# Kernel optimization log

Measured on AMD Instinct MI355X. Metric: run time of the kernel, lower is better.

## Reference

```python
import jax, jax.numpy as jnp
import numpy as np

BATCH, QLEN, KVLEN = 4, 8, 512
C, H = 512, 8
N = C // H  # 64
D_W, D_A, D_V, D_G = 32, 32, 32, 96
GN_EPS = 1e-5 * 8 ** 2  # head_size_divisor = 8


def setup_inputs() -> dict:
    key = jax.random.key(0)
    ks = jax.random.split(key, 32)
    rn = lambda i, sh, s=1.0: jax.random.normal(ks[i], sh, dtype=jnp.float32) * s
    ru = lambda i, sh: jax.random.uniform(ks[i], sh, dtype=jnp.float32)
    s = C ** -0.5
    return {
        "query": rn(0, (BATCH, QLEN, C)),
        "keyval": rn(1, (BATCH, KVLEN, C)),
        "v_first": rn(2, (BATCH * QLEN, KVLEN, C)),
        "x_r": ru(3, (1, 1, C)), "x_w": ru(4, (1, 1, C)), "x_k": ru(5, (1, 1, C)),
        "x_v": ru(6, (1, 1, C)), "x_a": ru(7, (1, 1, C)), "x_g": ru(8, (1, 1, C)),
        "w0": jnp.linspace(-7.0, -2.0, C, dtype=jnp.float32).reshape(1, 1, C) + 0.5,
        "w1": rn(9, (C, D_W), 0.02), "w2": rn(10, (D_W, C), 0.02),
        "a0": rn(11, (1, 1, C), 0.01), "a1": rn(12, (C, D_A), 0.02), "a2": rn(13, (D_A, C), 0.02),
        "v0": jnp.ones((1, 1, C), jnp.float32), "v1": rn(14, (C, D_V), 0.02), "v2": rn(15, (D_V, C), 0.02),
        "g1": rn(16, (C, D_G), 0.02), "g2": rn(17, (D_G, C), 0.02),
        "k_k": 0.85 + rn(18, (1, 1, C), 0.02), "k_a": jnp.ones((1, 1, C), jnp.float32),
        "r_k": rn(19, (H, N), 0.02),
        "Wr": rn(20, (C, C), 0.5 * s), "Wk": rn(21, (C, C), 0.05 * s),
        "Wv": rn(22, (C, C), 0.5 * s), "Wo": rn(23, (C, C), s),
        "ln_w": 1.0 + rn(24, (C,), 0.02), "ln_b": rn(25, (C,), 0.02),
    }


def _rwkv7_scan(r, w, k, v, a, b):
    # r,w,k,v,a,b: [B,T,C]; RWKV7 generalized delta rule, state [B,H,N,N] (value x key).
    B, T, _ = r.shape
    toTBHN = lambda t: t.reshape(B, T, H, N).transpose(1, 0, 2, 3)  # [T,B,H,N]
    rT, kT, vT, aT, bT = map(toTBHN, (r, k, v, a, b))
    wT = jnp.exp(-jnp.exp(toTBHN(w)))  # decay in (0,1)

    def step(state, xs):
        r_t, w_t, k_t, v_t, a_t, b_t = xs
        sa = jnp.einsum('bhij,bhj->bhi', state, a_t)  # state @ a
        state = (state * w_t[:, :, None, :]
                 + sa[..., None] * b_t[:, :, None, :]
                 + v_t[..., None] * k_t[:, :, None, :])
        out = jnp.einsum('bhij,bhj->bhi', state, r_t)
        return state, out

    state0 = jnp.zeros((B, H, N, N), dtype=jnp.float32)
    _, outs = jax.lax.scan(step, state0, (rT, wT, kT, vT, aT, bT))
    return outs.transpose(1, 0, 2, 3).reshape(B, T, C)  # [B,T,C]


def _forward(query, keyval, v_first, x_r, x_w, x_k, x_v, x_a, x_g,
             w0, w1, w2, a0, a1, a2, v0, v1, v2, g1, g2,
             k_k, k_a, r_k, Wr, Wk, Wv, Wo, ln_w, ln_b):
    batch, qlen, Cc = query.shape
    kvlen = keyval.shape[1]
    # cross-product expansion: every (query token, keyval sequence) pair
    eq = jnp.repeat(query[:, :, None, :], kvlen, axis=2).reshape(-1, kvlen, Cc)
    ek = jnp.repeat(keyval[:, None, :, :], qlen, axis=1).reshape(-1, kvlen, Cc)
    B, T = ek.shape[0], kvlen
    xx_cross = eq - ek
    shifted = jnp.pad(ek, ((0, 0), (1, 0), (0, 0)))[:, :-1]  # time_shift
    xx_kv = shifted - ek
    x = ek
    xr = x + xx_cross * x_r
    xw = x + xx_cross * x_w
    xa = x + xx_cross * x_a
    xg = x + xx_cross * x_g
    xk = x + xx_kv * x_k
    xv = x + xx_kv * x_v

    r = xr @ Wr
    w = -jax.nn.softplus(-(w0 + jnp.tanh(xw @ w1) @ w2)) - 0.5
    k = xk @ Wk
    v = xv @ Wv
    v = v + (v_first - v) * jax.nn.sigmoid(v0 + (xv @ v1) @ v2)  # layer_id != 0
    a = jax.nn.sigmoid(a0 + (xa @ a1) @ a2)
    g = jax.nn.sigmoid(xg @ g1) @ g2

    kk = k * k_k
    kkh = kk.reshape(B, T, H, N)
    kkh = kkh / jnp.maximum(jnp.linalg.norm(kkh, axis=-1, keepdims=True), 1e-12)
    kk = kkh.reshape(B, T, Cc)
    k = k * (1.0 + (a - 1.0) * k_a)

    xo = _rwkv7_scan(r, w, k, v, -kk, kk * a)

    # GroupNorm over H groups of N channels, eps = 1e-5 * head_size_divisor^2
    y = xo.reshape(B * T, H, N)
    mu = y.mean(axis=-1, keepdims=True)
    var = y.var(axis=-1, keepdims=True)
    yn = (y - mu) * jax.lax.rsqrt(var + GN_EPS)
    xo = (yn.reshape(B * T, Cc) * ln_w + ln_b).reshape(B, T, Cc)

    rk = (r.reshape(B, T, H, N) * k.reshape(B, T, H, N) * r_k).sum(axis=-1, keepdims=True)
    xo = xo + (rk * v.reshape(B, T, H, N)).reshape(B, T, Cc)
    xo = xo * g
    xo = xo[:, -1, :]  # frames=None path
    xo = xo.reshape(batch, qlen, Cc) @ Wo
    return xo, v_first


def reference(query, keyval, v_first, x_r, x_w, x_k, x_v, x_a, x_g,
              w0, w1, w2, a0, a1, a2, v0, v1, v2, g1, g2,
              k_k, k_a, r_k, Wr, Wk, Wv, Wo, ln_w, ln_b):
    return _forward(query, keyval, v_first, x_r, x_w, x_k, x_v, x_a, x_g,
                    w0, w1, w2, a0, a1, a2, v0, v1, v2, g1, g2,
                    k_k, k_a, r_k, Wr, Wk, Wv, Wo, ln_w, ln_b)
```

## Files before the change

### kernel.cpp

```cpp
#include <hip/hip_runtime.h>
#include <cstdint>

#define TT 512
#define CC 512
#define HH 8
#define NN 64
#define BQ 32
#define NB 4
#define TG 128

__device__ __forceinline__ float sigm(float x){ return 1.f/(1.f+__expf(-x)); }

__device__ __forceinline__ float wsum(float x){
  #pragma unroll
  for (int o=32;o;o>>=1) x += __shfl_xor(x, o, 64);
  return x;
}

template<int NR>
__device__ __forceinline__ void rowsum64_batch(float* x){
  #pragma unroll
  for (int i=0;i<NR;i++)
    x[i] += __int_as_float(__builtin_amdgcn_mov_dpp(__float_as_int(x[i]), 0x121, 0xf, 0xf, true));
  #pragma unroll
  for (int i=0;i<NR;i++)
    x[i] += __int_as_float(__builtin_amdgcn_mov_dpp(__float_as_int(x[i]), 0x122, 0xf, 0xf, true));
  #pragma unroll
  for (int i=0;i<NR;i++)
    x[i] += __int_as_float(__builtin_amdgcn_mov_dpp(__float_as_int(x[i]), 0x124, 0xf, 0xf, true));
  #pragma unroll
  for (int i=0;i<NR;i++)
    x[i] += __int_as_float(__builtin_amdgcn_mov_dpp(__float_as_int(x[i]), 0x128, 0xf, 0xf, true));
  float y[NR];
  #pragma unroll
  for (int i=0;i<NR;i++) asm("v_mov_b32 %0, %1" : "=v"(y[i]) : "v"(x[i]));
  #pragma unroll
  for (int i=0;i<NR;i++) asm("v_permlane16_swap_b32 %0, %1" : "+v"(x[i]), "+v"(y[i]));
  #pragma unroll
  for (int i=0;i<NR;i++) x[i] += y[i];
  #pragma unroll
  for (int i=0;i<NR;i++) asm("v_mov_b32 %0, %1" : "=v"(y[i]) : "v"(x[i]));
  #pragma unroll
  for (int i=0;i<NR;i++) asm("v_permlane32_swap_b32 %0, %1" : "+v"(x[i]), "+v"(y[i]));
  #pragma unroll
  for (int i=0;i<NR;i++) x[i] += y[i];
}

__global__ __launch_bounds__(256) void k_prep(
  const float* __restrict__ q, const float* __restrict__ kv,
  const float* __restrict__ x_r, const float* __restrict__ x_w,
  const float* __restrict__ x_a, const float* __restrict__ x_g,
  const float* __restrict__ w1, const float* __restrict__ a1,
  const float* __restrict__ g1,
  float* __restrict__ Qw, float* __restrict__ Qa,
  float* __restrict__ ghw, float* __restrict__ xrw)
{
  int bq = blockIdx.x, b = bq >> 3, tid = threadIdx.x;
  int wave = tid >> 6, lane = tid & 63;
  __shared__ float qxw[CC], qxa[CC], sxg[CC];
  for (int c = tid; c < CC; c += 256){
    float qv = q[bq*CC + c];
    float kl = kv[((size_t)b*TT + (TT-1))*CC + c];
    xrw[bq*CC + c] = kl + (qv - kl)*x_r[c];
    sxg[c] = kl + (qv - kl)*x_g[c];
    qxw[c] = qv*x_w[c];
    qxa[c] = qv*x_a[c];
  }
  __syncthreads();
  for (int dot = wave; dot < 160; dot += 4){
    const float* buf; const float* W; int ld, dd;
    if (dot < 32)      { buf = qxw; W = w1; ld = 32; dd = dot; }
    else if (dot < 64) { buf = qxa; W = a1; ld = 32; dd = dot-32; }
    else               { buf = sxg; W = g1; ld = 96; dd = dot-64; }
    float s = 0.f;
    #pragma unroll
    for (int m = 0; m < 8; m++){
      int c = m*64 + lane;
      s = fmaf(buf[c], W[c*ld + dd], s);
    }
    s = wsum(s);
    if (lane == 0){
      if (dot < 32)      Qw[bq*32 + dd] = s;
      else if (dot < 64) Qa[bq*32 + dd] = s;
      else               ghw[bq*96 + dd] = sigm(s);
    }
  }
}

__global__ __launch_bounds__(256) void k_rg(
  const float* __restrict__ xrw, const float* __restrict__ ghw,
  const float* __restrict__ Wr, const float* __restrict__ g2,
  float* __restrict__ rrow, float* __restrict__ grow)
{
  int bq = blockIdx.y; int co0 = blockIdx.x*64;
  int tid = threadIdx.x, tx = tid & 63, ty = tid >> 6;
  __shared__ float sxr[CC];
  __shared__ float sgh[96];
  __shared__ float red[4][64];
  sxr[tid]     = xrw[bq*CC + tid];
  sxr[tid+256] = xrw[bq*CC + tid + 256];
  if (tid < 96) sgh[tid] = ghw[bq*96 + tid];
  __syncthreads();
  float p = 0.f;
  for (int i = 0; i < 128; i++){
    int c = ty*128 + i;
    p = fmaf(sxr[c], Wr[(size_t)c*CC + co0 + tx], p);
  }
  red[ty][tx] = p;
  float pg = 0.f;
  for (int d = ty*24; d < ty*24 + 24; d++)
    pg = fmaf(sgh[d], g2[(size_t)d*CC + co0 + tx], pg);
  __syncthreads();
  if (ty == 0)
    rrow[bq*CC + co0 + tx] = (red[0][tx]+red[1][tx])+(red[2][tx]+red[3][tx]);
  __syncthreads();
  red[ty][tx] = pg;
  __syncthreads();
  if (ty == 0)
    grow[bq*CC + co0 + tx] = (red[0][tx]+red[1][tx])+(red[2][tx]+red[3][tx]);
}

__global__ __launch_bounds__(256) void k_shift(
  const float* __restrict__ kv, const float* __restrict__ x_k,
  const float* __restrict__ x_v,
  float* __restrict__ xk, float* __restrict__ xv)
{
  int g = blockIdx.x*256 + threadIdx.x;
  int bt = g >> 7, t = bt & (TT-1), c4 = g & 127;
  const float4* kv4 = (const float4*)kv;
  float4 cur = kv4[g];
  float4 sh  = t ? kv4[g-128] : make_float4(0.f,0.f,0.f,0.f);
  float4 kc  = ((const float4*)x_k)[c4];
  float4 vc  = ((const float4*)x_v)[c4];
  float4 ok, ov;
  ok.x = cur.x + (sh.x-cur.x)*kc.x; ov.x = cur.x + (sh.x-cur.x)*vc.x;
  ok.y = cur.y + (sh.y-cur.y)*kc.y; ov.y = cur.y + (sh.y-cur.y)*vc.y;
  ok.z = cur.z + (sh.z-cur.z)*kc.z; ov.z = cur.z + (sh.z-cur.z)*vc.z;
  ok.w = cur.w + (sh.w-cur.w)*kc.w; ov.w = cur.w + (sh.w-cur.w)*vc.w;
  ((float4*)xk)[g] = ok;
  ((float4*)xv)[g] = ov;
}

__global__ __launch_bounds__(256) void k_pgemm(
  const float* __restrict__ kv, const float* __restrict__ xv,
  const float* __restrict__ x_w, const float* __restrict__ x_a,
  const float* __restrict__ w1, const float* __restrict__ a1,
  const float* __restrict__ v1,
  float* __restrict__ Pw, float* __restrict__ Pa, float* __restrict__ HV)
{
  int mat = blockIdx.y;
  int r0 = blockIdx.x * 64;
  const float* A = (mat == 2) ? xv : kv;
  const float* B = (mat == 0) ? w1 : (mat == 1) ? a1 : v1;
  float* O       = (mat == 0) ? Pw : (mat == 1) ? Pa : HV;
  int tid = threadIdx.x;
  __shared__ float As[32][65];
  __shared__ float Bs[32][32];
  __shared__ float scl[CC];
  for (int c = tid; c < CC; c += 256)
    scl[c] = (mat == 0) ? (1.f - x_w[c]) : (mat == 1) ? (1.f - x_a[c]) : 1.f;
  __syncthreads();
  int tx = tid & 31, ty = tid >> 5;
  float acc[8];
  #pragma unroll
  for (int i = 0; i < 8; i++) acc[i] = 0.f;
  for (int k0 = 0; k0 < 512; k0 += 32){
    #pragma unroll
    for (int p = 0; p < 8; p++){
      int e = tid + p*256;
      int kk2 = e & 31, r = e >> 5;
      As[kk2][r] = A[(size_t)(r0+r)*512 + k0 + kk2] * scl[k0 + kk2];
    }
    #pragma unroll
    for (int p = 0; p < 4; p++){
      int e = tid + p*256;
      int n = e & 31, kk2 = e >> 5;
      Bs[kk2][n] = B[(size_t)(k0+kk2)*32 + n];
    }
    __syncthreads();
    #pragma unroll
    for (int kk2 = 0; kk2 < 32; kk2++){
      float bb = Bs[kk2][tx];
      #pragma unroll
      for (int i = 0; i < 8; i++)
        acc[i] = fmaf(As[kk2][ty*8 + i], bb, acc[i]);
    }
    __syncthreads();
  }
  #pragma unroll
  for (int i = 0; i < 8; i++)
    O[(size_t)(r0 + ty*8 + i)*32 + tx] = acc[i];
}

__global__ __launch_bounds__(256) void gemm2(
  const float* __restrict__ A0, const float* __restrict__ W0, float* __restrict__ kgP,
  const float* __restrict__ A1, const float* __restrict__ W1, float* __restrict__ vpP)
{
  __shared__ float As[32][68];
  __shared__ float Bs[32][64];
  int z = blockIdx.z;
  const float* A = z ? A1 : A0;
  const float* W = z ? W1 : W0;
  int tid = threadIdx.x;
  int tx = tid & 15, ty = tid >> 4;
  int m0 = blockIdx.y*64, n0 = blockIdx.x*64;
  float acc[4][4];
  #pragma unroll
  for (int i=0;i<4;i++)
    #pragma unroll
    for (int j=0;j<4;j++) acc[i][j]=0.f;

  for (int k0 = 0; k0 < 512; k0 += 32){
    #pragma unroll
    for (int i = 0; i < 8; i++){
      int e = tid + i*256;
      int kk = e & 31, m = e >> 5;
      As[kk][m] = A[(size_t)(m0+m)*512 + k0 + kk];
    }
    #pragma unroll
    for (int i = 0; i < 8; i++){
      int e = tid + i*256;
      int n = e & 63, kk = e >> 6;
      Bs[kk][n] = W[(size_t)(k0+kk)*512 + n0 + n];
    }
    __syncthreads();
    #pragma unroll
    for (int kk = 0; kk < 32; kk++){
      float a4[4], b4[4];
      #pragma unroll
      for (int i=0;i<4;i++) a4[i] = As[kk][ty*4+i];
      #pragma unroll
      for (int j=0;j<4;j++) b4[j] = Bs[kk][tx*4+j];
      #pragma unroll
      for (int i=0;i<4;i++)
        #pragma unroll
        for (int j=0;j<4;j++) acc[i][j] += a4[i]*b4[j];
    }
    __syncthreads();
  }
  int m = m0 + ty*4;
  int b = m >> 9, t = m & (TT-1), tg = t >> 2;
  int h = n0 >> 6;
  float* dstB = z ? vpP : kgP;
  float4* dst = (float4*)dstB + ((size_t)(b*HH + h)*TG + tg)*64 + tx*4;
  #pragma unroll
  for (int j=0;j<4;j++)
    dst[j] = make_float4(acc[0][j],acc[1][j],acc[2][j],acc[3][j]);
}

__global__ __launch_bounds__(512) void k_svn(
  const float* __restrict__ HV, const float* __restrict__ v2,
  const float* __restrict__ v0, const float* __restrict__ k_k,
  const float* __restrict__ kgP,
  float* __restrict__ svP, float* __restrict__ kkP)
{
  int blk = blockIdx.x;
  int b = blk >> 7, tg = blk & (TG-1);
  int tid = threadIdx.x;
  __shared__ float hv[4][32];
  if (tid < 128){
    int u = tid >> 5, d = tid & 31;
    hv[u][d] = HV[((size_t)(b*TT + tg*4 + u))*32 + d];
  }
  __syncthreads();
  int c = tid, h = c >> 6, cc0 = c & 63;
  size_t o = ((size_t)(b*HH + h)*TG + tg)*64 + cc0;
  float4 kg4 = ((const float4*)kgP)[o];
  float kkc = k_k[c];
  float q0 = kg4.x*kkc, q1 = kg4.y*kkc, q2 = kg4.z*kkc, q3 = kg4.w*kkc;
  float ss[4] = {q0*q0, q1*q1, q2*q2, q3*q3};
  rowsum64_batch<4>(ss);
  float4 kkq;
  kkq.x = q0 / fmaxf(sqrtf(ss[0]), 1e-12f);
  kkq.y = q1 / fmaxf(sqrtf(ss[1]), 1e-12f);
  kkq.z = q2 / fmaxf(sqrtf(ss[2]), 1e-12f);
  kkq.w = q3 / fmaxf(sqrtf(ss[3]), 1e-12f);
  ((float4*)kkP)[o] = kkq;
  float v0c = v0[c];
  float s0 = v0c, s1 = v0c, s2 = v0c, s3 = v0c;
  #pragma unroll
  for (int d = 0; d < 32; d++){
    float vc = v2[d*CC + c];
    s0 = fmaf(hv[0][d], vc, s0);
    s1 = fmaf(hv[1][d], vc, s1);
    s2 = fmaf(hv[2][d], vc, s2);
    s3 = fmaf(hv[3][d], vc, s3);
  }
  ((float4*)svP)[o] = make_float4(sigm(s0), sigm(s1), sigm(s2), sigm(s3));
}

__global__ __launch_bounds__(512) void k_wa(
  const float* __restrict__ Pw, const float* __restrict__ Pa,
  const float* __restrict__ Qw, const float* __restrict__ Qa,
  const float* __restrict__ w2, const float* __restrict__ a2,
  const float* __restrict__ w0, const float* __restrict__ a0,
  float* __restrict__ wP, float* __restrict__ aP)
{
  int blk = blockIdx.x;
  int bq = blk >> 7, tg = blk & (TG-1), t0 = tg*4, b = bq >> 3;
  int tid = threadIdx.x;
  __shared__ float sth[4][32], sal[4][32];
  if (tid < 256){
    int g = (tid >> 5) & 3, d = tid & 31;
    int pidx = ((b << 9) | (t0 + g))*32 + d;
    if (tid < 128) sth[g][d] = tanhf(Pw[pidx] + Qw[bq*32 + d]);
    else           sal[g][d] = Pa[pidx] + Qa[bq*32 + d];
  }
  __syncthreads();
  int c = tid, h = c >> 6, cc0 = c & 63;
  float wreg[32], areg[32];
  #pragma unroll
  for (int d = 0; d < 32; d++){ wreg[d] = w2[d*CC + c]; areg[d] = a2[d*CC + c]; }
  float w0c = w0[c], a0c = a0[c];
  float w4a[4], a4a[4];
  #pragma unroll
  for (int g = 0; g < 4; g++){
    float wa = 0.f, aa = 0.f;
    #pragma unroll
    for (int d = 0; d < 32; d++){
      wa = fmaf(sth[g][d], wreg[d], wa);
      aa = fmaf(sal[g][d], areg[d], aa);
    }
    w4a[g] = __expf(-0.60653066f * sigm(w0c + wa));
    a4a[g] = sigm(a0c + aa);
  }
  size_t o = ((size_t)(bq*HH + h)*TG + tg)*64 + cc0;
  ((float4*)wP)[o] = make_float4(w4a[0],w4a[1],w4a[2],w4a[3]);
  ((float4*)aP)[o] = make_float4(a4a[0],a4a[1],a4a[2],a4a[3]);
}

#define SCAN_PAIR(wh,ah,gh,nh,vh, wl,al,gl,nl,vl) do{ \
  float kh = (gh)*fmaf((ah)-1.f, kac, 1.f), bh = (nh)*(ah); \
  float klo = (gl)*fmaf((al)-1.f, kac, 1.f), blo = (nl)*(al); \
  float u = (wh)*g; \
  float dd[6]; \
  dd[0]=kh*g; dd[1]=bh*g; dd[2]=klo*u; dd[3]=blo*u; dd[4]=klo*(nh); dd[5]=blo*(nh); \
  rowsum64_batch<6>(dd); \
  out = fmaf(dd[0], (vh), out); \
  g   = fmaf(-dd[1], (nh), u); \
  out = fmaf(fmaf(-dd[4], dd[1], dd[2]), (vl), out); \
  g   = fmaf(-fmaf(-dd[5], dd[1], dd[3]), (nl), (wl)*g); \
}while(0)

__global__ __launch_bounds__(64, 1) void k_scan(
  const float* __restrict__ wP, const float* __restrict__ aP,
  const float* __restrict__ kgP, const float* __restrict__ kkP,
  const float* __restrict__ vpP, const float* __restrict__ svP,
  const float* __restrict__ vfirst,
  const float* __restrict__ rrow, const float* __restrict__ grow,
  const float* __restrict__ r_k, const float* __restrict__ k_a,
  const float* __restrict__ ln_w, const float* __restrict__ ln_b,
  float* __restrict__ xo)
{
  int blk = blockIdx.x; int bq = blk >> 3, h = blk & 7, b = bq >> 3;
  int lane = threadIdx.x & 63;

  const float4* wp4 = (const float4*)wP  + ((size_t)(bq*HH + h))*TG*64 + lane;
  const float4* ap4 = (const float4*)aP  + ((size_t)(bq*HH + h))*TG*64 + lane;
  const float4* gp4 = (const float4*)kgP + ((size_t)(b*HH + h))*TG*64 + lane;
  const float4* np4 = (const float4*)kkP + ((size_t)(b*HH + h))*TG*64 + lane;
  const float4* pp4 = (const float4*)vpP + ((size_t)(b*HH + h))*TG*64 + lane;
  const float4* sp4 = (const float4*)svP + ((size_t)(b*HH + h))*TG*64 + lane;
  const float*  pvf = vfirst + (size_t)bq*TT*CC + h*NN + lane;

  float kac = k_a[h*NN + lane];
  float g   = rrow[(size_t)bq*CC + h*NN + lane];
  float out = 0.f;

  constexpr int PD = 4;
  float4 fw[PD], fa[PD], fg[PD], fn[PD], fp[PD], fs[PD];
  float fv0[PD], fv1[PD], fv2[PD], fv3[PD];
  #pragma unroll
  for (int d = 0; d < PD; ++d){
    int gg = TG-1 - d; int go = gg*64;
    fw[d]=wp4[go]; fa[d]=ap4[go]; fg[d]=gp4[go]; fn[d]=np4[go];
    fp[d]=pp4[go]; fs[d]=sp4[go];
    const float* pv = pvf + (size_t)(4*gg)*CC;
    fv0[d]=pv[0]; fv1[d]=pv[CC]; fv2[d]=pv[2*CC]; fv3[d]=pv[3*CC];
  }

  #pragma unroll 1
  for (int gb = 0; gb < TG; gb += PD){
    #pragma unroll
    for (int sl = 0; sl < PD; ++sl){
      int gi = TG-1 - (gb + sl);
      float4 w4=fw[sl], a4=fa[sl], g4=fg[sl], n4=fn[sl], p4=fp[sl], s4=fs[sl];
      float x3=fv3[sl], x2=fv2[sl], x1=fv1[sl], x0=fv0[sl];
      int gp = gi - PD; gp = gp < 0 ? 0 : gp; int go = gp*64;
      fw[sl]=wp4[go]; fa[sl]=ap4[go]; fg[sl]=gp4[go]; fn[sl]=np4[go];
      fp[sl]=pp4[go]; fs[sl]=sp4[go];
      { const float* pv = pvf + (size_t)(4*gp)*CC;
        fv0[sl]=pv[0]; fv1[sl]=pv[CC]; fv2[sl]=pv[2*CC]; fv3[sl]=pv[3*CC]; }
      __builtin_amdgcn_sched_barrier(0);
      float v3 = fmaf(x3 - p4.w, s4.w, p4.w);
      float v2_ = fmaf(x2 - p4.z, s4.z, p4.z);
      float v1_ = fmaf(x1 - p4.y, s4.y, p4.y);
      float v0_ = fmaf(x0 - p4.x, s4.x, p4.x);
      SCAN_PAIR(w4.w,a4.w,g4.w,n4.w,v3,  w4.z,a4.z,g4.z,n4.z,v2_);
      SCAN_PAIR(w4.y,a4.y,g4.y,n4.y,v1_, w4.x,a4.x,g4.x,n4.x,v0_);
    }
  }

  {
    float mean = wsum(out) * (1.f/NN);
    float dv = out - mean;
    float var = wsum(dv*dv) * (1.f/NN);
    float yn = dv * rsqrtf(var + 6.4e-4f);
    int c = h*NN + lane;
    float y2 = yn * ln_w[c] + ln_b[c];
    int goT = (TG-1)*64;
    float4 kgT = gp4[goT]; float4 aT = ap4[goT];
    float kl  = kgT.w * fmaf(aT.w - 1.f, kac, 1.f);
    float rl  = rrow[(size_t)bq*CC + c];
    float rk  = wsum(rl*kl*r_k[c]);
    float vp_ = pp4[goT].w, sv_ = sp4[goT].w;
    float vf_ = pvf[(size_t)(TT-1)*CC];
    float v_i = fmaf(vf_ - vp_, sv_, vp_);
    float res = (y2 + rk*v_i) * grow[(size_t)bq*CC + c];
    xo[bq*CC + c] = res;
  }
}

__global__ __launch_bounds__(256) void k_out(
  const float* __restrict__ xo, const float* __restrict__ Wo,
  float* __restrict__ outp)
{
  int bq = blockIdx.y; int co0 = blockIdx.x*64;
  int tid = threadIdx.x, tx = tid & 63, ty = tid >> 6;
  __shared__ float row[CC];
  __shared__ float red[4][64];
  row[tid]     = xo[bq*CC + tid];
  row[tid+256] = xo[bq*CC + tid + 256];
  __syncthreads();
  float p = 0.f;
  for (int i = 0; i < 128; i++){
    int c = ty*128 + i;
    p = fmaf(row[c], Wo[(size_t)c*CC + co0 + tx], p);
  }
  red[ty][tx] = p;
  __syncthreads();
  if (ty == 0)
    outp[bq*CC + co0 + tx] = (red[0][tx]+red[1][tx])+(red[2][tx]+red[3][tx]);
}

extern "C" void kernel_launch(void* const* d_in, const int* in_sizes, int n_in,
                              void* d_out, int out_size, void* d_ws, size_t ws_size,
                              hipStream_t stream)
{
  const float* q   = (const float*)d_in[0];
  const float* kv  = (const float*)d_in[1];
  const float* vf  = (const float*)d_in[2];
  const float* x_r = (const float*)d_in[3];
  const float* x_w = (const float*)d_in[4];
  const float* x_k = (const float*)d_in[5];
  const float* x_v = (const float*)d_in[6];
  const float* x_a = (const float*)d_in[7];
  const float* x_g = (const float*)d_in[8];
  const float* w0  = (const float*)d_in[9];
  const float* w1  = (const float*)d_in[10];
  const float* w2  = (const float*)d_in[11];
  const float* a0  = (const float*)d_in[12];
  const float* a1  = (const float*)d_in[13];
  const float* a2  = (const float*)d_in[14];
  const float* v0  = (const float*)d_in[15];
  const float* v1  = (const float*)d_in[16];
  const float* v2  = (const float*)d_in[17];
  const float* g1  = (const float*)d_in[18];
  const float* g2  = (const float*)d_in[19];
  const float* k_k = (const float*)d_in[20];
  const float* k_a = (const float*)d_in[21];
  const float* r_k = (const float*)d_in[22];
  const float* Wr  = (const float*)d_in[23];
  const float* Wk  = (const float*)d_in[24];
  const float* Wv  = (const float*)d_in[25];
  const float* Wo  = (const float*)d_in[26];
  const float* lnw = (const float*)d_in[27];
  const float* lnb = (const float*)d_in[28];
  float* outp = (float*)d_out;
  float* ws = (float*)d_ws;

  float* xk  = ws + 0;
  float* xv  = ws + 1048576;
  float* kgP = ws + 2097152;
  float* vpP = ws + 3145728;
  float* svP = ws + 4194304;
  float* kkP = ws + 5242880;
  float* Pw  = ws + 6291456;
  float* Pa  = ws + 6356992;
  float* Qw  = ws + 6422528;
  float* Qa  = ws + 6423552;
  float* HV  = ws + 6424576;
  float* rr  = ws + 7473152;
  float* gr  = ws + 7489536;
  float* xo  = ws + 7505920;
  float* wP  = ws + 7522304;
  float* aP  = ws + 15910912;
  float* xrw = ws + 32688128;
  float* ghw = ws + 32704512;

  hipMemcpyAsync(outp + BQ*CC, vf,
                 (size_t)BQ*TT*CC*sizeof(float), hipMemcpyDeviceToDevice, stream);

  k_prep<<<32, 256, 0, stream>>>(q, kv, x_r, x_w, x_a, x_g, w1, a1, g1,
                                 Qw, Qa, ghw, xrw);
  k_rg<<<dim3(8, 32), 256, 0, stream>>>(xrw, ghw, Wr, g2, rr, gr);
  k_shift<<<1024, 256, 0, stream>>>(kv, x_k, x_v, xk, xv);
  gemm2<<<dim3(8, 32, 2), 256, 0, stream>>>(xk, Wk, kgP, xv, Wv, vpP);
  k_pgemm<<<dim3(32, 3), 256, 0, stream>>>(kv, xv, x_w, x_a, w1, a1, v1,
                                           Pw, Pa, HV);
  k_svn<<<NB*TG, 512, 0, stream>>>(HV, v2, v0, k_k, kgP, svP, kkP);
  k_wa<<<BQ*TG, 512, 0, stream>>>(Pw, Pa, Qw, Qa, w2, a2, w0, a0, wP, aP);
  k_scan<<<BQ*HH, 64, 0, stream>>>(wP, aP, kgP, kkP, vpP, svP, vf, rr, gr,
                                   r_k, k_a, lnw, lnb, xo);
  k_out<<<dim3(8, 32), 256, 0, stream>>>(xo, Wo, outp);
}
```

Measured before the change: 369.2 us.

## Pack two scan chains per wave with two channels per lane

Measured after the change: 374.3 us. Within noise of the previous version (+1.4%).

```diff
diff --git a/kernel.cpp b/kernel.cpp
--- a/kernel.cpp
+++ b/kernel.cpp
@@ -17,6 +17,12 @@
   return x;
 }
 
+__device__ __forceinline__ float wsum32(float x){
+  #pragma unroll
+  for (int o=16;o;o>>=1) x += __shfl_xor(x, o, 64);
+  return x;
+}
+
 template<int NR>
 __device__ __forceinline__ void rowsum64_batch(float* x){
   #pragma unroll
@@ -42,6 +48,29 @@
   for (int i=0;i<NR;i++) asm("v_mov_b32 %0, %1" : "=v"(y[i]) : "v"(x[i]));
   #pragma unroll
   for (int i=0;i<NR;i++) asm("v_permlane32_swap_b32 %0, %1" : "+v"(x[i]), "+v"(y[i]));
+  #pragma unroll
+  for (int i=0;i<NR;i++) x[i] += y[i];
+}
+
+template<int NR>
+__device__ __forceinline__ void rowsum32_batch(float* x){
+  #pragma unroll
+  for (int i=0;i<NR;i++)
+    x[i] += __int_as_float(__builtin_amdgcn_mov_dpp(__float_as_int(x[i]), 0x121, 0xf, 0xf, true));
+  #pragma unroll
+  for (int i=0;i<NR;i++)
+    x[i] += __int_as_float(__builtin_amdgcn_mov_dpp(__float_as_int(x[i]), 0x122, 0xf, 0xf, true));
+  #pragma unroll
+  for (int i=0;i<NR;i++)
+    x[i] += __int_as_float(__builtin_amdgcn_mov_dpp(__float_as_int(x[i]), 0x124, 0xf, 0xf, true));
+  #pragma unroll
+  for (int i=0;i<NR;i++)
+    x[i] += __int_as_float(__builtin_amdgcn_mov_dpp(__float_as_int(x[i]), 0x128, 0xf, 0xf, true));
+  float y[NR];
+  #pragma unroll
+  for (int i=0;i<NR;i++) asm("v_mov_b32 %0, %1" : "=v"(y[i]) : "v"(x[i]));
+  #pragma unroll
+  for (int i=0;i<NR;i++) asm("v_permlane16_swap_b32 %0, %1" : "+v"(x[i]), "+v"(y[i]));
   #pragma unroll
   for (int i=0;i<NR;i++) x[i] += y[i];
 }
@@ -329,17 +358,23 @@
   ((float4*)aP)[o] = make_float4(a4a[0],a4a[1],a4a[2],a4a[3]);
 }
 
-#define SCAN_PAIR(wh,ah,gh,nh,vh, wl,al,gl,nl,vl) do{ \
-  float kh = (gh)*fmaf((ah)-1.f, kac, 1.f), bh = (nh)*(ah); \
-  float klo = (gl)*fmaf((al)-1.f, kac, 1.f), blo = (nl)*(al); \
-  float u = (wh)*g; \
-  float dd[6]; \
-  dd[0]=kh*g; dd[1]=bh*g; dd[2]=klo*u; dd[3]=blo*u; dd[4]=klo*(nh); dd[5]=blo*(nh); \
-  rowsum64_batch<6>(dd); \
-  out = fmaf(dd[0], (vh), out); \
-  g   = fmaf(-dd[1], (nh), u); \
-  out = fmaf(fmaf(-dd[4], dd[1], dd[2]), (vl), out); \
-  g   = fmaf(-fmaf(-dd[5], dd[1], dd[3]), (nl), (wl)*g); \
+#define SCAN_STEP2(CMP, u) do{ \
+  float cw0=w4a.CMP, cw1=w4b.CMP, ca0=a4a.CMP, ca1=a4b.CMP; \
+  float cg0=g4a.CMP, cg1=g4b.CMP, cn0=n4a.CMP, cn1=n4b.CMP; \
+  float cp0=p4a.CMP, cp1=p4b.CMP, cs0=s4a.CMP, cs1=s4b.CMP; \
+  float v0_ = fmaf(vfl[u]-cp0, cs0, cp0); \
+  float v1_ = fmaf(vfl[4+u]-cp1, cs1, cp1); \
+  float k0_ = cg0*fmaf(ca0-1.f, kac0, 1.f); \
+  float k1_ = cg1*fmaf(ca1-1.f, kac1, 1.f); \
+  float b0_ = cn0*ca0, b1_ = cn1*ca1; \
+  float rr[2]; \
+  rr[0] = fmaf(k1_, g1, k0_*g0); \
+  rr[1] = fmaf(b1_, g1, b0_*g0); \
+  rowsum32_batch<2>(rr); \
+  out0 = fmaf(rr[0], v0_, out0); \
+  out1 = fmaf(rr[0], v1_, out1); \
+  g0 = fmaf(cw0, g0, -(cn0*rr[1])); \
+  g1 = fmaf(cw1, g1, -(cn1*rr[1])); \
 }while(0)
 
 __global__ __launch_bounds__(64, 1) void k_scan(
@@ -352,31 +387,43 @@
   const float* __restrict__ ln_w, const float* __restrict__ ln_b,
   float* __restrict__ xo)
 {
-  int blk = blockIdx.x; int bq = blk >> 3, h = blk & 7, b = bq >> 3;
   int lane = threadIdx.x & 63;
-
-  const float4* wp4 = (const float4*)wP  + ((size_t)(bq*HH + h))*TG*64 + lane;
-  const float4* ap4 = (const float4*)aP  + ((size_t)(bq*HH + h))*TG*64 + lane;
-  const float4* gp4 = (const float4*)kgP + ((size_t)(b*HH + h))*TG*64 + lane;
-  const float4* np4 = (const float4*)kkP + ((size_t)(b*HH + h))*TG*64 + lane;
-  const float4* pp4 = (const float4*)vpP + ((size_t)(b*HH + h))*TG*64 + lane;
-  const float4* sp4 = (const float4*)svP + ((size_t)(b*HH + h))*TG*64 + lane;
-  const float*  pvf = vfirst + (size_t)bq*TT*CC + h*NN + lane;
-
-  float kac = k_a[h*NN + lane];
-  float g   = rrow[(size_t)bq*CC + h*NN + lane];
-  float out = 0.f;
-
-  constexpr int PD = 4;
-  float4 fw[PD], fa[PD], fg[PD], fn[PD], fp[PD], fs[PD];
-  float fv0[PD], fv1[PD], fv2[PD], fv3[PD];
+  int half = lane >> 5, li = lane & 31;
+  int chain = blockIdx.x*2 + half;
+  int bq = chain >> 3, h = chain & 7, b = bq >> 3;
+  int c0 = 2*li;
+  int ch0 = h*NN + c0;
+
+  size_t bhq = ((size_t)(bq*HH + h))*TG*64 + c0;
+  size_t bh  = ((size_t)(b *HH + h))*TG*64 + c0;
+  const float4* wp4 = (const float4*)wP  + bhq;
+  const float4* ap4 = (const float4*)aP  + bhq;
+  const float4* gp4 = (const float4*)kgP + bh;
+  const float4* np4 = (const float4*)kkP + bh;
+  const float4* pp4 = (const float4*)vpP + bh;
+  const float4* sp4 = (const float4*)svP + bh;
+  const float*  pvf = vfirst + (size_t)bq*TT*CC + ch0;
+
+  float kac0 = k_a[ch0], kac1 = k_a[ch0+1];
+  float g0 = rrow[(size_t)bq*CC + ch0];
+  float g1 = rrow[(size_t)bq*CC + ch0 + 1];
+  float out0 = 0.f, out1 = 0.f;
+
+  constexpr int PD = 2;
+  float4 fw[PD][2], fa[PD][2], fg[PD][2], fn[PD][2], fp[PD][2], fs[PD][2];
+  float  fvf[PD][8];
   #pragma unroll
   for (int d = 0; d < PD; ++d){
     int gg = TG-1 - d; int go = gg*64;
-    fw[d]=wp4[go]; fa[d]=ap4[go]; fg[d]=gp4[go]; fn[d]=np4[go];
-    fp[d]=pp4[go]; fs[d]=sp4[go];
+    fw[d][0]=wp4[go]; fw[d][1]=wp4[go+1];
+    fa[d][0]=ap4[go]; fa[d][1]=ap4[go+1];
+    fg[d][0]=gp4[go]; fg[d][1]=gp4[go+1];
+    fn[d][0]=np4[go]; fn[d][1]=np4[go+1];
+    fp[d][0]=pp4[go]; fp[d][1]=pp4[go+1];
+    fs[d][0]=sp4[go]; fs[d][1]=sp4[go+1];
     const float* pv = pvf + (size_t)(4*gg)*CC;
-    fv0[d]=pv[0]; fv1[d]=pv[CC]; fv2[d]=pv[2*CC]; fv3[d]=pv[3*CC];
+    #pragma unroll
+    for (int u = 0; u < 4; ++u){ fvf[d][u] = pv[(size_t)u*CC]; fvf[d][4+u] = pv[(size_t)u*CC + 1]; }
   }
 
   #pragma unroll 1
@@ -384,40 +431,53 @@
     #pragma unroll
     for (int sl = 0; sl < PD; ++sl){
       int gi = TG-1 - (gb + sl);
-      float4 w4=fw[sl], a4=fa[sl], g4=fg[sl], n4=fn[sl], p4=fp[sl], s4=fs[sl];
-      float x3=fv3[sl], x2=fv2[sl], x1=fv1[sl], x0=fv0[sl];
+      float4 w4a=fw[sl][0], w4b=fw[sl][1], a4a=fa[sl][0], a4b=fa[sl][1];
+      float4 g4a=fg[sl][0], g4b=fg[sl][1], n4a=fn[sl][0], n4b=fn[sl][1];
+      float4 p4a=fp[sl][0], p4b=fp[sl][1], s4a=fs[sl][0], s4b=fs[sl][1];
+      float vfl[8];
+      #pragma unroll
+      for (int u = 0; u < 8; ++u) vfl[u] = fvf[sl][u];
       int gp = gi - PD; gp = gp < 0 ? 0 : gp; int go = gp*64;
-      fw[sl]=wp4[go]; fa[sl]=ap4[go]; fg[sl]=gp4[go]; fn[sl]=np4[go];
-      fp[sl]=pp4[go]; fs[sl]=sp4[go];
+      fw[sl][0]=wp4[go]; fw[sl][1]=wp4[go+1];
+      fa[sl][0]=ap4[go]; fa[sl][1]=ap4[go+1];
+      fg[sl][0]=gp4[go]; fg[sl][1]=gp4[go+1];
+      fn[sl][0]=np4[go]; fn[sl][1]=np4[go+1];
+      fp[sl][0]=pp4[go]; fp[sl][1]=pp4[go+1];
+      fs[sl][0]=sp4[go]; fs[sl][1]=sp4[go+1];
       { const float* pv = pvf + (size_t)(4*gp)*CC;
-        fv0[sl]=pv[0]; fv1[sl]=pv[CC]; fv2[sl]=pv[2*CC]; fv3[sl]=pv[3*CC]; }
+        #pragma unroll
+        for (int u = 0; u < 4; ++u){ fvf[sl][u] = pv[(size_t)u*CC]; fvf[sl][4+u] = pv[(size_t)u*CC + 1]; } }
       __builtin_amdgcn_sched_barrier(0);
-      float v3 = fmaf(x3 - p4.w, s4.w, p4.w);
-      float v2_ = fmaf(x2 - p4.z, s4.z, p4.z);
-      float v1_ = fmaf(x1 - p4.y, s4.y, p4.y);
-      float v0_ = fmaf(x0 - p4.x, s4.x, p4.x);
-      SCAN_PAIR(w4.w,a4.w,g4.w,n4.w,v3,  w4.z,a4.z,g4.z,n4.z,v2_);
-      SCAN_PAIR(w4.y,a4.y,g4.y,n4.y,v1_, w4.x,a4.x,g4.x,n4.x,v0_);
+      SCAN_STEP2(w, 3);
+      SCAN_STEP2(z, 2);
+      SCAN_STEP2(y, 1);
+      SCAN_STEP2(x, 0);
     }
   }
 
   {
-    float mean = wsum(out) * (1.f/NN);
-    float dv = out - mean;
-    float var = wsum(dv*dv) * (1.f/NN);
-    float yn = dv * rsqrtf(var + 6.4e-4f);
-    int c = h*NN + lane;
-    float y2 = yn * ln_w[c] + ln_b[c];
+    float mean = wsum32(out0 + out1) * (1.f/NN);
+    float dv0 = out0 - mean, dv1 = out1 - mean;
+    float var = wsum32(dv0*dv0 + dv1*dv1) * (1.f/NN);
+    float inv = rsqrtf(var + 6.4e-4f);
+    float y20 = dv0*inv * ln_w[ch0]   + ln_b[ch0];
+    float y21 = dv1*inv * ln_w[ch0+1] + ln_b[ch0+1];
     int goT = (TG-1)*64;
-    float4 kgT = gp4[goT]; float4 aT = ap4[goT];
-    float kl  = kgT.w * fmaf(aT.w - 1.f, kac, 1.f);
-    float rl  = rrow[(size_t)bq*CC + c];
-    float rk  = wsum(rl*kl*r_k[c]);
-    float vp_ = pp4[goT].w, sv_ = sp4[goT].w;
-    float vf_ = pvf[(size_t)(TT-1)*CC];
-    float v_i = fmaf(vf_ - vp_, sv_, vp_);
-    float res = (y2 + rk*v_i) * grow[(size_t)bq*CC + c];
-    xo[bq*CC + c] = res;
+    float4 kgT0 = gp4[goT], kgT1 = gp4[goT+1];
+    float4 aT0  = ap4[goT], aT1  = ap4[goT+1];
+    float kl0 = kgT0.w * fmaf(aT0.w - 1.f, kac0, 1.f);
+    float kl1 = kgT1.w * fmaf(aT1.w - 1.f, kac1, 1.f);
+    float rl0 = rrow[(size_t)bq*CC + ch0], rl1 = rrow[(size_t)bq*CC + ch0+1];
+    float rk = wsum32(fmaf(rl1*kl1, r_k[ch0+1], rl0*kl0*r_k[ch0]));
+    float4 pT0 = pp4[goT], pT1 = pp4[goT+1];
+    float4 sT0 = sp4[goT], sT1 = sp4[goT+1];
+    float vfT0 = pvf[(size_t)(TT-1)*CC], vfT1 = pvf[(size_t)(TT-1)*CC + 1];
+    float vi0 = fmaf(vfT0 - pT0.w, sT0.w, pT0.w);
+    float vi1 = fmaf(vfT1 - pT1.w, sT1.w, pT1.w);
+    float r0 = (y20 + rk*vi0) * grow[(size_t)bq*CC + ch0];
+    float r1 = (y21 + rk*vi1) * grow[(size_t)bq*CC + ch0+1];
+    xo[(size_t)bq*CC + ch0]     = r0;
+    xo[(size_t)bq*CC + ch0 + 1] = r1;
   }
 }
 
@@ -510,7 +570,7 @@
                                            Pw, Pa, HV);
   k_svn<<<NB*TG, 512, 0, stream>>>(HV, v2, v0, k_k, kgP, svP, kkP);
   k_wa<<<BQ*TG, 512, 0, stream>>>(Pw, Pa, Qw, Qa, w2, a2, w0, a0, wP, aP);
-  k_scan<<<BQ*HH, 64, 0, stream>>>(wP, aP, kgP, kkP, vpP, svP, vf, rr, gr,
-                                   r_k, k_a, lnw, lnb, xo);
+  k_scan<<<BQ*HH/2, 64, 0, stream>>>(wP, aP, kgP, kkP, vpP, svP, vf, rr, gr,
+                                     r_k, k_a, lnw, lnb, xo);
   k_out<<<dim3(8, 32), 256, 0, stream>>>(xo, Wo, outp);
 }
```

## Fuse token-shift into GEMMs and precompute k,b for simpler scan step

Applied to the files above, without the earlier changes.

New measurement: 411.9 us. 1.12x slower.

```diff
diff --git a/kernel.cpp b/kernel.cpp
--- a/kernel.cpp
+++ b/kernel.cpp
@@ -120,45 +120,27 @@
     grow[bq*CC + co0 + tx] = (red[0][tx]+red[1][tx])+(red[2][tx]+red[3][tx]);
 }
 
-__global__ __launch_bounds__(256) void k_shift(
-  const float* __restrict__ kv, const float* __restrict__ x_k,
+__global__ __launch_bounds__(256) void k_pgemm(
+  const float* __restrict__ kv,
+  const float* __restrict__ x_w, const float* __restrict__ x_a,
   const float* __restrict__ x_v,
-  float* __restrict__ xk, float* __restrict__ xv)
-{
-  int g = blockIdx.x*256 + threadIdx.x;
-  int bt = g >> 7, t = bt & (TT-1), c4 = g & 127;
-  const float4* kv4 = (const float4*)kv;
-  float4 cur = kv4[g];
-  float4 sh  = t ? kv4[g-128] : make_float4(0.f,0.f,0.f,0.f);
-  float4 kc  = ((const float4*)x_k)[c4];
-  float4 vc  = ((const float4*)x_v)[c4];
-  float4 ok, ov;
-  ok.x = cur.x + (sh.x-cur.x)*kc.x; ov.x = cur.x + (sh.x-cur.x)*vc.x;
-  ok.y = cur.y + (sh.y-cur.y)*kc.y; ov.y = cur.y + (sh.y-cur.y)*vc.y;
-  ok.z = cur.z + (sh.z-cur.z)*kc.z; ov.z = cur.z + (sh.z-cur.z)*vc.z;
-  ok.w = cur.w + (sh.w-cur.w)*kc.w; ov.w = cur.w + (sh.w-cur.w)*vc.w;
-  ((float4*)xk)[g] = ok;
-  ((float4*)xv)[g] = ov;
-}
-
-__global__ __launch_bounds__(256) void k_pgemm(
-  const float* __restrict__ kv, const float* __restrict__ xv,
-  const float* __restrict__ x_w, const float* __restrict__ x_a,
   const float* __restrict__ w1, const float* __restrict__ a1,
   const float* __restrict__ v1,
   float* __restrict__ Pw, float* __restrict__ Pa, float* __restrict__ HV)
 {
   int mat = blockIdx.y;
   int r0 = blockIdx.x * 64;
-  const float* A = (mat == 2) ? xv : kv;
   const float* B = (mat == 0) ? w1 : (mat == 1) ? a1 : v1;
   float* O       = (mat == 0) ? Pw : (mat == 1) ? Pa : HV;
   int tid = threadIdx.x;
   __shared__ float As[32][65];
   __shared__ float Bs[32][32];
   __shared__ float scl[CC];
-  for (int c = tid; c < CC; c += 256)
+  __shared__ float xm[CC];
+  for (int c = tid; c < CC; c += 256){
     scl[c] = (mat == 0) ? (1.f - x_w[c]) : (mat == 1) ? (1.f - x_a[c]) : 1.f;
+    xm[c]  = (mat == 2) ? x_v[c] : 0.f;
+  }
   __syncthreads();
   int tx = tid & 31, ty = tid >> 5;
   float acc[8];
@@ -169,7 +151,11 @@
     for (int p = 0; p < 8; p++){
       int e = tid + p*256;
       int kk2 = e & 31, r = e >> 5;
-      As[kk2][r] = A[(size_t)(r0+r)*512 + k0 + kk2] * scl[k0 + kk2];
+      int m = r0 + r, col = k0 + kk2;
+      float cur = kv[(size_t)m*512 + col];
+      int t = m & (TT-1);
+      float sh = t ? kv[(size_t)(m-1)*512 + col] : 0.f;
+      As[kk2][r] = fmaf(sh - cur, xm[col], cur) * scl[col];
     }
     #pragma unroll
     for (int p = 0; p < 4; p++){
@@ -193,15 +179,21 @@
 }
 
 __global__ __launch_bounds__(256) void gemm2(
-  const float* __restrict__ A0, const float* __restrict__ W0, float* __restrict__ kgP,
-  const float* __restrict__ A1, const float* __restrict__ W1, float* __restrict__ vpP)
+  const float* __restrict__ kv,
+  const float* __restrict__ x_k, const float* __restrict__ Wk,
+  float* __restrict__ kgP,
+  const float* __restrict__ x_v, const float* __restrict__ Wv,
+  float* __restrict__ vpP)
 {
   __shared__ float As[32][68];
   __shared__ float Bs[32][64];
+  __shared__ float xm[CC];
   int z = blockIdx.z;
-  const float* A = z ? A1 : A0;
-  const float* W = z ? W1 : W0;
+  const float* W = z ? Wv : Wk;
+  const float* xmix = z ? x_v : x_k;
   int tid = threadIdx.x;
+  for (int c = tid; c < CC; c += 256) xm[c] = xmix[c];
+  __syncthreads();
   int tx = tid & 15, ty = tid >> 4;
   int m0 = blockIdx.y*64, n0 = blockIdx.x*64;
   float acc[4][4];
@@ -214,8 +206,12 @@
     #pragma unroll
     for (int i = 0; i < 8; i++){
       int e = tid + i*256;
-      int kk = e & 31, m = e >> 5;
-      As[kk][m] = A[(size_t)(m0+m)*512 + k0 + kk];
+      int kk = e & 31, mm = e >> 5;
+      int m = m0 + mm, col = k0 + kk;
+      float cur = kv[(size_t)m*512 + col];
+      int t = m & (TT-1);
+      float sh = t ? kv[(size_t)(m-1)*512 + col] : 0.f;
+      As[kk][mm] = fmaf(sh - cur, xm[col], cur);
     }
     #pragma unroll
     for (int i = 0; i < 8; i++){
@@ -289,12 +285,14 @@
   ((float4*)svP)[o] = make_float4(sigm(s0), sigm(s1), sigm(s2), sigm(s3));
 }
 
-__global__ __launch_bounds__(512) void k_wa(
+__global__ __launch_bounds__(512) void k_wkb(
   const float* __restrict__ Pw, const float* __restrict__ Pa,
   const float* __restrict__ Qw, const float* __restrict__ Qa,
   const float* __restrict__ w2, const float* __restrict__ a2,
   const float* __restrict__ w0, const float* __restrict__ a0,
-  float* __restrict__ wP, float* __restrict__ aP)
+  const float* __restrict__ k_a,
+  const float* __restrict__ kgP, const float* __restrict__ kkP,
+  float* __restrict__ wP, float* __restrict__ kP, float* __restrict__ bP)
 {
   int blk = blockIdx.x;
   int bq = blk >> 7, tg = blk & (TG-1), t0 = tg*4, b = bq >> 3;
@@ -311,8 +309,13 @@
   float wreg[32], areg[32];
   #pragma unroll
   for (int d = 0; d < 32; d++){ wreg[d] = w2[d*CC + c]; areg[d] = a2[d*CC + c]; }
-  float w0c = w0[c], a0c = a0[c];
-  float w4a[4], a4a[4];
+  float w0c = w0[c], a0c = a0[c], kac = k_a[c];
+  size_t ob = ((size_t)(b*HH + h)*TG + tg)*64 + cc0;
+  float4 kg4 = ((const float4*)kgP)[ob];
+  float4 kk4 = ((const float4*)kkP)[ob];
+  float kga[4] = {kg4.x, kg4.y, kg4.z, kg4.w};
+  float kka[4] = {kk4.x, kk4.y, kk4.z, kk4.w};
+  float w4a[4], k4a[4], b4a[4];
   #pragma unroll
   for (int g = 0; g < 4; g++){
     float wa = 0.f, aa = 0.f;
@@ -321,59 +324,54 @@
       wa = fmaf(sth[g][d], wreg[d], wa);
       aa = fmaf(sal[g][d], areg[d], aa);
     }
+    float a_sig = sigm(a0c + aa);
     w4a[g] = __expf(-0.60653066f * sigm(w0c + wa));
-    a4a[g] = sigm(a0c + aa);
+    k4a[g] = kga[g]*(1.f + (a_sig - 1.f)*kac);
+    b4a[g] = kka[g]*a_sig;
   }
   size_t o = ((size_t)(bq*HH + h)*TG + tg)*64 + cc0;
   ((float4*)wP)[o] = make_float4(w4a[0],w4a[1],w4a[2],w4a[3]);
-  ((float4*)aP)[o] = make_float4(a4a[0],a4a[1],a4a[2],a4a[3]);
-}
-
-#define SCAN_PAIR(wh,ah,gh,nh,vh, wl,al,gl,nl,vl) do{ \
-  float kh = (gh)*fmaf((ah)-1.f, kac, 1.f), bh = (nh)*(ah); \
-  float klo = (gl)*fmaf((al)-1.f, kac, 1.f), blo = (nl)*(al); \
-  float u = (wh)*g; \
-  float dd[6]; \
-  dd[0]=kh*g; dd[1]=bh*g; dd[2]=klo*u; dd[3]=blo*u; dd[4]=klo*(nh); dd[5]=blo*(nh); \
-  rowsum64_batch<6>(dd); \
-  out = fmaf(dd[0], (vh), out); \
-  g   = fmaf(-dd[1], (nh), u); \
-  out = fmaf(fmaf(-dd[4], dd[1], dd[2]), (vl), out); \
-  g   = fmaf(-fmaf(-dd[5], dd[1], dd[3]), (nl), (wl)*g); \
-}while(0)
+  ((float4*)kP)[o] = make_float4(k4a[0],k4a[1],k4a[2],k4a[3]);
+  ((float4*)bP)[o] = make_float4(b4a[0],b4a[1],b4a[2],b4a[3]);
+}
+
+#define SCAN_STEP(wc,kc,bc,ac,pc,sc,vfc) do{ \
+  float vj = fmaf((vfc)-(pc), (sc), (pc)); \
+  float rr[2]; rr[0]=(kc)*g; rr[1]=(bc)*g; \
+  rowsum64_batch<2>(rr); \
+  out = fmaf(rr[0], vj, out); \
+  g = fmaf((wc), g, -((ac)*rr[1])); }while(0)
 
 __global__ __launch_bounds__(64, 1) void k_scan(
-  const float* __restrict__ wP, const float* __restrict__ aP,
-  const float* __restrict__ kgP, const float* __restrict__ kkP,
+  const float* __restrict__ wP, const float* __restrict__ kP,
+  const float* __restrict__ bP, const float* __restrict__ kkP,
   const float* __restrict__ vpP, const float* __restrict__ svP,
   const float* __restrict__ vfirst,
   const float* __restrict__ rrow, const float* __restrict__ grow,
-  const float* __restrict__ r_k, const float* __restrict__ k_a,
-  const float* __restrict__ ln_w, const float* __restrict__ ln_b,
-  float* __restrict__ xo)
+  const float* __restrict__ r_k, const float* __restrict__ ln_w,
+  const float* __restrict__ ln_b, float* __restrict__ xo)
 {
   int blk = blockIdx.x; int bq = blk >> 3, h = blk & 7, b = bq >> 3;
   int lane = threadIdx.x & 63;
 
   const float4* wp4 = (const float4*)wP  + ((size_t)(bq*HH + h))*TG*64 + lane;
-  const float4* ap4 = (const float4*)aP  + ((size_t)(bq*HH + h))*TG*64 + lane;
-  const float4* gp4 = (const float4*)kgP + ((size_t)(b*HH + h))*TG*64 + lane;
-  const float4* np4 = (const float4*)kkP + ((size_t)(b*HH + h))*TG*64 + lane;
+  const float4* kp4 = (const float4*)kP  + ((size_t)(bq*HH + h))*TG*64 + lane;
+  const float4* bp4 = (const float4*)bP  + ((size_t)(bq*HH + h))*TG*64 + lane;
+  const float4* ap4 = (const float4*)kkP + ((size_t)(b*HH + h))*TG*64 + lane;
   const float4* pp4 = (const float4*)vpP + ((size_t)(b*HH + h))*TG*64 + lane;
   const float4* sp4 = (const float4*)svP + ((size_t)(b*HH + h))*TG*64 + lane;
   const float*  pvf = vfirst + (size_t)bq*TT*CC + h*NN + lane;
 
-  float kac = k_a[h*NN + lane];
   float g   = rrow[(size_t)bq*CC + h*NN + lane];
   float out = 0.f;
 
   constexpr int PD = 4;
-  float4 fw[PD], fa[PD], fg[PD], fn[PD], fp[PD], fs[PD];
+  float4 fw[PD], fk[PD], fb[PD], fa[PD], fp[PD], fs[PD];
   float fv0[PD], fv1[PD], fv2[PD], fv3[PD];
   #pragma unroll
   for (int d = 0; d < PD; ++d){
     int gg = TG-1 - d; int go = gg*64;
-    fw[d]=wp4[go]; fa[d]=ap4[go]; fg[d]=gp4[go]; fn[d]=np4[go];
+    fw[d]=wp4[go]; fk[d]=kp4[go]; fb[d]=bp4[go]; fa[d]=ap4[go];
     fp[d]=pp4[go]; fs[d]=sp4[go];
     const float* pv = pvf + (size_t)(4*gg)*CC;
     fv0[d]=pv[0]; fv1[d]=pv[CC]; fv2[d]=pv[2*CC]; fv3[d]=pv[3*CC];
@@ -384,20 +382,18 @@
     #pragma unroll
     for (int sl = 0; sl < PD; ++sl){
       int gi = TG-1 - (gb + sl);
-      float4 w4=fw[sl], a4=fa[sl], g4=fg[sl], n4=fn[sl], p4=fp[sl], s4=fs[sl];
-      float x3=fv3[sl], x2=fv2[sl], x1=fv1[sl], x0=fv0[sl];
+      float4 w4=fw[sl], k4=fk[sl], b4=fb[sl], a4=fa[sl], p4=fp[sl], s4=fs[sl];
+      float v3=fv3[sl], v2_=fv2[sl], v1_=fv1[sl], v0_=fv0[sl];
       int gp = gi - PD; gp = gp < 0 ? 0 : gp; int go = gp*64;
-      fw[sl]=wp4[go]; fa[sl]=ap4[go]; fg[sl]=gp4[go]; fn[sl]=np4[go];
+      fw[sl]=wp4[go]; fk[sl]=kp4[go]; fb[sl]=bp4[go]; fa[sl]=ap4[go];
       fp[sl]=pp4[go]; fs[sl]=sp4[go];
       { const float* pv = pvf + (size_t)(4*gp)*CC;
         fv0[sl]=pv[0]; fv1[sl]=pv[CC]; fv2[sl]=pv[2*CC]; fv3[sl]=pv[3*CC]; }
       __builtin_amdgcn_sched_barrier(0);
-      float v3 = fmaf(x3 - p4.w, s4.w, p4.w);
-      float v2_ = fmaf(x2 - p4.z, s4.z, p4.z);
-      float v1_ = fmaf(x1 - p4.y, s4.y, p4.y);
-      float v0_ = fmaf(x0 - p4.x, s4.x, p4.x);
-      SCAN_PAIR(w4.w,a4.w,g4.w,n4.w,v3,  w4.z,a4.z,g4.z,n4.z,v2_);
-      SCAN_PAIR(w4.y,a4.y,g4.y,n4.y,v1_, w4.x,a4.x,g4.x,n4.x,v0_);
+      SCAN_STEP(w4.w,k4.w,b4.w,a4.w,p4.w,s4.w,v3);
+      SCAN_STEP(w4.z,k4.z,b4.z,a4.z,p4.z,s4.z,v2_);
+      SCAN_STEP(w4.y,k4.y,b4.y,a4.y,p4.y,s4.y,v1_);
+      SCAN_STEP(w4.x,k4.x,b4.x,a4.x,p4.x,s4.x,v0_);
     }
   }
 
@@ -409,8 +405,7 @@
     int c = h*NN + lane;
     float y2 = yn * ln_w[c] + ln_b[c];
     int goT = (TG-1)*64;
-    float4 kgT = gp4[goT]; float4 aT = ap4[goT];
-    float kl  = kgT.w * fmaf(aT.w - 1.f, kac, 1.f);
+    float kl  = kp4[goT].w;
     float rl  = rrow[(size_t)bq*CC + c];
     float rk  = wsum(rl*kl*r_k[c]);
     float vp_ = pp4[goT].w, sv_ = sp4[goT].w;
@@ -479,8 +474,6 @@
   float* outp = (float*)d_out;
   float* ws = (float*)d_ws;
 
-  float* xk  = ws + 0;
-  float* xv  = ws + 1048576;
   float* kgP = ws + 2097152;
   float* vpP = ws + 3145728;
   float* svP = ws + 4194304;
@@ -494,7 +487,8 @@
   float* gr  = ws + 7489536;
   float* xo  = ws + 7505920;
   float* wP  = ws + 7522304;
-  float* aP  = ws + 15910912;
+  float* kP  = ws + 15910912;
+  float* bP  = ws + 24299520;
   float* xrw = ws + 32688128;
   float* ghw = ws + 32704512;
 
@@ -504,13 +498,13 @@
   k_prep<<<32, 256, 0, stream>>>(q, kv, x_r, x_w, x_a, x_g, w1, a1, g1,
                                  Qw, Qa, ghw, xrw);
   k_rg<<<dim3(8, 32), 256, 0, stream>>>(xrw, ghw, Wr, g2, rr, gr);
-  k_shift<<<1024, 256, 0, stream>>>(kv, x_k, x_v, xk, xv);
-  gemm2<<<dim3(8, 32, 2), 256, 0, stream>>>(xk, Wk, kgP, xv, Wv, vpP);
-  k_pgemm<<<dim3(32, 3), 256, 0, stream>>>(kv, xv, x_w, x_a, w1, a1, v1,
+  gemm2<<<dim3(8, 32, 2), 256, 0, stream>>>(kv, x_k, Wk, kgP, x_v, Wv, vpP);
+  k_pgemm<<<dim3(32, 3), 256, 0, stream>>>(kv, x_w, x_a, x_v, w1, a1, v1,
                                            Pw, Pa, HV);
   k_svn<<<NB*TG, 512, 0, stream>>>(HV, v2, v0, k_k, kgP, svP, kkP);
-  k_wa<<<BQ*TG, 512, 0, stream>>>(Pw, Pa, Qw, Qa, w2, a2, w0, a0, wP, aP);
-  k_scan<<<BQ*HH, 64, 0, stream>>>(wP, aP, kgP, kkP, vpP, svP, vf, rr, gr,
-                                   r_k, k_a, lnw, lnb, xo);
+  k_wkb<<<BQ*TG, 512, 0, stream>>>(Pw, Pa, Qw, Qa, w2, a2, w0, a0, k_a,
+                                   kgP, kkP, wP, kP, bP);
+  k_scan<<<BQ*HH, 64, 0, stream>>>(wP, kP, bP, kkP, vpP, svP, vf, rr, gr, r_k,
+                                   lnw, lnb, xo);
   k_out<<<dim3(8, 32), 256, 0, stream>>>(xo, Wo, outp);
 }
```

## Fuse v_first copy into scan kernel and simplify scan step to single-timestep updates

Applied to the files above, without the earlier changes.

New measurement: 347.9 us. -5.8%, faster.

```diff
diff --git a/kernel.cpp b/kernel.cpp
--- a/kernel.cpp
+++ b/kernel.cpp
@@ -329,18 +329,14 @@
   ((float4*)aP)[o] = make_float4(a4a[0],a4a[1],a4a[2],a4a[3]);
 }
 
-#define SCAN_PAIR(wh,ah,gh,nh,vh, wl,al,gl,nl,vl) do{ \
-  float kh = (gh)*fmaf((ah)-1.f, kac, 1.f), bh = (nh)*(ah); \
-  float klo = (gl)*fmaf((al)-1.f, kac, 1.f), blo = (nl)*(al); \
-  float u = (wh)*g; \
-  float dd[6]; \
-  dd[0]=kh*g; dd[1]=bh*g; dd[2]=klo*u; dd[3]=blo*u; dd[4]=klo*(nh); dd[5]=blo*(nh); \
-  rowsum64_batch<6>(dd); \
-  out = fmaf(dd[0], (vh), out); \
-  g   = fmaf(-dd[1], (nh), u); \
-  out = fmaf(fmaf(-dd[4], dd[1], dd[2]), (vl), out); \
-  g   = fmaf(-fmaf(-dd[5], dd[1], dd[3]), (nl), (wl)*g); \
-}while(0)
+#define SCAN_STEP(wc,ac,gc,nc,pc,sc,vfc) do{ \
+  float vj = fmaf((vfc)-(pc), (sc), (pc)); \
+  float kc = (gc)*fmaf((ac)-1.f, kac, 1.f); \
+  float bc = (nc)*(ac); \
+  float rr[2]; rr[0]=kc*g; rr[1]=bc*g; \
+  rowsum64_batch<2>(rr); \
+  out = fmaf(rr[0], vj, out); \
+  g = fmaf((wc), g, -((nc)*rr[1])); }while(0)
 
 __global__ __launch_bounds__(64, 1) void k_scan(
   const float* __restrict__ wP, const float* __restrict__ aP,
@@ -350,7 +346,7 @@
   const float* __restrict__ rrow, const float* __restrict__ grow,
   const float* __restrict__ r_k, const float* __restrict__ k_a,
   const float* __restrict__ ln_w, const float* __restrict__ ln_b,
-  float* __restrict__ xo)
+  float* __restrict__ xo, float* __restrict__ vf_out)
 {
   int blk = blockIdx.x; int bq = blk >> 3, h = blk & 7, b = bq >> 3;
   int lane = threadIdx.x & 63;
@@ -362,6 +358,7 @@
   const float4* pp4 = (const float4*)vpP + ((size_t)(b*HH + h))*TG*64 + lane;
   const float4* sp4 = (const float4*)svP + ((size_t)(b*HH + h))*TG*64 + lane;
   const float*  pvf = vfirst + (size_t)bq*TT*CC + h*NN + lane;
+  float*        pvo = vf_out + (size_t)bq*TT*CC + h*NN + lane;
 
   float kac = k_a[h*NN + lane];
   float g   = rrow[(size_t)bq*CC + h*NN + lane];
@@ -385,19 +382,21 @@
     for (int sl = 0; sl < PD; ++sl){
       int gi = TG-1 - (gb + sl);
       float4 w4=fw[sl], a4=fa[sl], g4=fg[sl], n4=fn[sl], p4=fp[sl], s4=fs[sl];
-      float x3=fv3[sl], x2=fv2[sl], x1=fv1[sl], x0=fv0[sl];
+      float v3=fv3[sl], v2_=fv2[sl], v1_=fv1[sl], v0_=fv0[sl];
       int gp = gi - PD; gp = gp < 0 ? 0 : gp; int go = gp*64;
       fw[sl]=wp4[go]; fa[sl]=ap4[go]; fg[sl]=gp4[go]; fn[sl]=np4[go];
       fp[sl]=pp4[go]; fs[sl]=sp4[go];
       { const float* pv = pvf + (size_t)(4*gp)*CC;
         fv0[sl]=pv[0]; fv1[sl]=pv[CC]; fv2[sl]=pv[2*CC]; fv3[sl]=pv[3*CC]; }
+      {
+        float* po = pvo + (size_t)(4*gi)*CC;
+        po[0] = v0_; po[CC] = v1_; po[2*CC] = v2_; po[3*CC] = v3;
+      }
       __builtin_amdgcn_sched_barrier(0);
-      float v3 = fmaf(x3 - p4.w, s4.w, p4.w);
-      float v2_ = fmaf(x2 - p4.z, s4.z, p4.z);
-      float v1_ = fmaf(x1 - p4.y, s4.y, p4.y);
-      float v0_ = fmaf(x0 - p4.x, s4.x, p4.x);
-      SCAN_PAIR(w4.w,a4.w,g4.w,n4.w,v3,  w4.z,a4.z,g4.z,n4.z,v2_);
-      SCAN_PAIR(w4.y,a4.y,g4.y,n4.y,v1_, w4.x,a4.x,g4.x,n4.x,v0_);
+      SCAN_STEP(w4.w,a4.w,g4.w,n4.w,p4.w,s4.w,v3);
+      SCAN_STEP(w4.z,a4.z,g4.z,n4.z,p4.z,s4.z,v2_);
+      SCAN_STEP(w4.y,a4.y,g4.y,n4.y,p4.y,s4.y,v1_);
+      SCAN_STEP(w4.x,a4.x,g4.x,n4.x,p4.x,s4.x,v0_);
     }
   }
 
@@ -409,8 +408,8 @@
     int c = h*NN + lane;
     float y2 = yn * ln_w[c] + ln_b[c];
     int goT = (TG-1)*64;
-    float4 kgT = gp4[goT]; float4 aT = ap4[goT];
-    float kl  = kgT.w * fmaf(aT.w - 1.f, kac, 1.f);
+    float kgT = gp4[goT].w, aT = ap4[goT].w;
+    float kl  = kgT * fmaf(aT - 1.f, kac, 1.f);
     float rl  = rrow[(size_t)bq*CC + c];
     float rk  = wsum(rl*kl*r_k[c]);
     float vp_ = pp4[goT].w, sv_ = sp4[goT].w;
@@ -498,9 +497,6 @@
   float* xrw = ws + 32688128;
   float* ghw = ws + 32704512;
 
-  hipMemcpyAsync(outp + BQ*CC, vf,
-                 (size_t)BQ*TT*CC*sizeof(float), hipMemcpyDeviceToDevice, stream);
-
   k_prep<<<32, 256, 0, stream>>>(q, kv, x_r, x_w, x_a, x_g, w1, a1, g1,
                                  Qw, Qa, ghw, xrw);
   k_rg<<<dim3(8, 32), 256, 0, stream>>>(xrw, ghw, Wr, g2, rr, gr);
@@ -511,6 +507,6 @@
   k_svn<<<NB*TG, 512, 0, stream>>>(HV, v2, v0, k_k, kgP, svP, kkP);
   k_wa<<<BQ*TG, 512, 0, stream>>>(Pw, Pa, Qw, Qa, w2, a2, w0, a0, wP, aP);
   k_scan<<<BQ*HH, 64, 0, stream>>>(wP, aP, kgP, kkP, vpP, svP, vf, rr, gr,
-                                   r_k, k_a, lnw, lnb, xo);
+                                   r_k, k_a, lnw, lnb, xo, outp + BQ*CC);
   k_out<<<dim3(8, 32), 256, 0, stream>>>(xo, Wo, outp);
 }
```
